# Optimization experiments

Measured on AMD Instinct MI355X. Metric: run time of the kernel, lower is better.

Reference implementation:

```python
import jax, jax.numpy as jnp
import numpy as np
from jax import lax

B, T, D = 2048, 300, 40
H = 64          # BasicLSTMCell num_units
D1 = 128        # dense1 units
OUT = 512       # out_dim (num speakers)
FORGET_BIAS = 1.0
BN_EPS = 1e-3   # tf.layers.BatchNormalization default


def setup_inputs() -> dict:
    key = jax.random.key(0)
    ks = jax.random.split(key, 10)
    X = jax.random.normal(ks[0], (B, T, D), dtype=jnp.float32)
    seq_length = jax.random.randint(ks[1], (B,), 1, T + 1).astype(jnp.int32)
    # BasicLSTMCell kernel: [input_dim + H, 4H], gate order i, j, f, o
    lstm_kernel = jax.random.normal(ks[2], (D + H, 4 * H), dtype=jnp.float32) * 0.08
    lstm_bias = jnp.zeros((4 * H,), dtype=jnp.float32)
    W1 = jax.random.normal(ks[3], (H, D1), dtype=jnp.float32) * 0.1
    b1 = jnp.zeros((D1,), dtype=jnp.float32)
    gamma = jnp.ones((D1,), dtype=jnp.float32)
    beta = jnp.zeros((D1,), dtype=jnp.float32)
    moving_mean = jnp.zeros((D1,), dtype=jnp.float32)
    moving_var = jnp.ones((D1,), dtype=jnp.float32)
    W2 = jax.random.normal(ks[4], (D1, OUT), dtype=jnp.float32) * 0.1
    b2 = jnp.zeros((OUT,), dtype=jnp.float32)
    return {"X": X, "seq_length": seq_length,
            "lstm_kernel": lstm_kernel, "lstm_bias": lstm_bias,
            "W1": W1, "b1": b1, "gamma": gamma, "beta": beta,
            "moving_mean": moving_mean, "moving_var": moving_var,
            "W2": W2, "b2": b2}


def reference(X, seq_length, lstm_kernel, lstm_bias, W1, b1, gamma, beta,
              moving_mean, moving_var, W2, b2):
    b = X.shape[0]
    c0 = jnp.zeros((b, H), dtype=X.dtype)
    h0 = jnp.zeros((b, H), dtype=X.dtype)

    def step(carry, x_t):
        c, h = carry
        z = jnp.concatenate([x_t, h], axis=1) @ lstm_kernel + lstm_bias
        i, j, f, o = jnp.split(z, 4, axis=1)
        new_c = c * jax.nn.sigmoid(f + FORGET_BIAS) + jax.nn.sigmoid(i) * jnp.tanh(j)
        new_h = jnp.tanh(new_c) * jax.nn.sigmoid(o)
        return (new_c, new_h), new_h

    _, outs = lax.scan(step, (c0, h0), jnp.swapaxes(X, 0, 1))  # [T, B, H]
    outs = jnp.swapaxes(outs, 0, 1)  # [B, T, H]

    # gather last valid timestep per sample
    idx = (seq_length - 1).astype(jnp.int32)
    final = jnp.take_along_axis(outs, idx[:, None, None], axis=1)[:, 0, :]  # [B, H]

    x = jax.nn.relu(final @ W1 + b1)
    # BatchNorm in inference mode (training=False): use moving statistics
    x = gamma * (x - moving_mean) * lax.rsqrt(moving_var + BN_EPS) + beta
    return jax.nn.softmax(x @ W2 + b2, axis=-1)
```

## Files before the change

### kernel.cpp

```cpp
#include <hip/hip_runtime.h>
#include <stdint.h>

#define TT 300
#define DD 40
#define SB 8
#define AROW 200
#define ZROW 260

typedef __attribute__((ext_vector_type(8))) short short8;
typedef __attribute__((ext_vector_type(4))) float f32x4;

__device__ __forceinline__ ushort f2bf(float f) {
  uint32_t b = __float_as_uint(f);
  b += 0x7FFFu + ((b >> 16) & 1u);
  return (ushort)(b >> 16);
}
__device__ __forceinline__ float sigm(float x) {
  return __builtin_amdgcn_rcpf(1.0f + __expf(-x));
}
__device__ __forceinline__ float tanh_f(float x) {
  return 1.0f - 2.0f * __builtin_amdgcn_rcpf(1.0f + __expf(2.0f * x));
}

__global__ __launch_bounds__(256, 1) void lstm_mfma_kernel(
    const float* __restrict__ X, const int* __restrict__ seqlen,
    const float* __restrict__ Wk, const float* __restrict__ bias,
    float* __restrict__ hfin)
{
  __shared__ ushort wstage[64 * 128];
  __shared__ ushort Ash[16 * AROW];
  __shared__ float zbuf[8 * ZROW];

  const int tid = threadIdx.x;
  const int wv = tid >> 6, lane = tid & 63;
  const int s0 = blockIdx.x * SB;

  for (int i = tid; i < 16 * AROW; i += 256) Ash[i] = 0;

  short8 Bf[6][4];
  for (int c = 0; c < 4; ++c) {
    __syncthreads();
    for (int i = tid; i < 64 * 128; i += 256) {
      int kp = i >> 6, cc = i & 63;
      ushort v = 0;
      int ks = (kp < 40) ? kp : ((kp >= 64) ? (kp - 24) : -1);
      if (ks >= 0) {
        int u = c * 16 + (cc >> 2), g = cc & 3;
        v = f2bf(Wk[ks * 256 + g * 64 + u]);
      }
      wstage[cc * 128 + kp] = v;
    }
    __syncthreads();
    if (wv == c) {
      #pragma unroll
      for (int kt = 0; kt < 6; ++kt) {
        int kk = ((kt < 4) ? kt * 32 : (kt * 32 - 64)) + (lane >> 4) * 8;
        #pragma unroll
        for (int nt = 0; nt < 4; ++nt) {
          int cc = nt * 16 + (lane & 15);
          Bf[kt][nt] = *reinterpret_cast<const short8*>(&wstage[cc * 128 + kk]);
        }
      }
    }
  }

  const int ps = tid >> 5;
  const int u0 = (2 * tid) & 63, u1 = u0 + 1;
  const int mylen = seqlen[s0 + ps];
  const float bi0 = bias[u0],      bj0 = bias[64 + u0];
  const float bfg0 = bias[128 + u0] + 1.0f, bo0 = bias[192 + u0];
  const float bi1 = bias[u1],      bj1 = bias[64 + u1];
  const float bfg1 = bias[128 + u1] + 1.0f, bo1 = bias[192 + u1];

  int ml = seqlen[s0 + (lane & 7)];
  #pragma unroll
  for (int off = 1; off < 64; off <<= 1) ml = max(ml, __shfl_xor(ml, off));

  const int iA = tid, iB = 256 + tid;
  const int sA = (iA * 205) >> 13, dA = iA - sA * 40;
  int sB = (iB * 205) >> 13; if (sB > 7) sB = 7;
  const int dB = iB - sB * 40;
  const float* xpA = X + (size_t)(s0 + sA) * (TT * DD) + dA;
  const float* xpB = X + (size_t)(s0 + sB) * (TT * DD) + dB;
  const bool hasB = (iB < SB * DD);

  Ash[sA * AROW + dA] = f2bf(xpA[0]);
  if (hasB) Ash[sB * AROW + dB] = f2bf(xpB[0]);
  __syncthreads();

  float c0 = 0.f, c1 = 0.f, hf0 = 0.f, hf1 = 0.f;

  for (int t = 0; t < ml; ++t) {
    short8 Af[6];
    #pragma unroll
    for (int kt = 0; kt < 6; ++kt)
      Af[kt] = *reinterpret_cast<const short8*>(
          &Ash[(lane & 15) * AROW + kt * 32 + (lane >> 4) * 8]);

    const bool pre = (t + 1 < ml);
    float xnA = 0.f, xnB = 0.f;
    if (pre) {
      xnA = xpA[(t + 1) * DD];
      if (hasB) xnB = xpB[(t + 1) * DD];
    }

    f32x4 zero4 = {0.f, 0.f, 0.f, 0.f};
    f32x4 acc[4] = {zero4, zero4, zero4, zero4};
    #pragma unroll
    for (int kt = 0; kt < 6; ++kt) {
      #pragma unroll
      for (int nt = 0; nt < 4; ++nt)
        acc[nt] = __builtin_amdgcn_mfma_f32_16x16x32_bf16(Af[kt], Bf[kt][nt], acc[nt], 0, 0, 0);
    }

    if (lane < 32) {
      const int q = lane >> 4, cl = lane & 15;
      #pragma unroll
      for (int nt = 0; nt < 4; ++nt) {
        #pragma unroll
        for (int r = 0; r < 4; ++r)
          zbuf[(q * 4 + r) * ZROW + wv * 64 + nt * 16 + cl] = acc[nt][r];
      }
    }
    __syncthreads();

    f32x4 z0 = *reinterpret_cast<const f32x4*>(&zbuf[ps * ZROW + u0 * 4]);
    f32x4 z1 = *reinterpret_cast<const f32x4*>(&zbuf[ps * ZROW + u1 * 4]);
    float nc0 = c0 * sigm(z0[2] + bfg0) + sigm(z0[0] + bi0) * tanh_f(z0[1] + bj0);
    float nh0 = tanh_f(nc0) * sigm(z0[3] + bo0);
    float nc1 = c1 * sigm(z1[2] + bfg1) + sigm(z1[0] + bi1) * tanh_f(z1[1] + bj1);
    float nh1 = tanh_f(nc1) * sigm(z1[3] + bo1);
    c0 = nc0; c1 = nc1;
    if (t == mylen - 1) { hf0 = nh0; hf1 = nh1; }

    ushort hh0 = f2bf(nh0);
    ushort hl0 = f2bf(nh0 - __uint_as_float((uint32_t)hh0 << 16));
    ushort hh1 = f2bf(nh1);
    ushort hl1 = f2bf(nh1 - __uint_as_float((uint32_t)hh1 << 16));
    Ash[ps * AROW + 64 + u0] = hh0;
    Ash[ps * AROW + 128 + u0] = hl0;
    Ash[ps * AROW + 64 + u1] = hh1;
    Ash[ps * AROW + 128 + u1] = hl1;
    if (pre) {
      Ash[sA * AROW + dA] = f2bf(xnA);
      if (hasB) Ash[sB * AROW + dB] = f2bf(xnB);
    }
    __syncthreads();
  }

  hfin[(size_t)(s0 + ps) * 64 + u0] = hf0;
  hfin[(size_t)(s0 + ps) * 64 + u1] = hf1;
}

__global__ __launch_bounds__(256, 1) void head_kernel(
    const float* __restrict__ hfin,
    const float* __restrict__ W1, const float* __restrict__ b1,
    const float* __restrict__ gamma, const float* __restrict__ beta,
    const float* __restrict__ mmean, const float* __restrict__ mvar,
    const float* __restrict__ W2, const float* __restrict__ b2,
    float* __restrict__ out)
{
  __shared__ float hl[16 * 64];
  __shared__ float d1t[128 * 20];
  __shared__ float lg[16 * 516];
  const int tid = threadIdx.x;
  const int b0 = blockIdx.x * 16;

  for (int i = tid; i < 16 * 64; i += 256) hl[i] = hfin[(size_t)b0 * 64 + i];
  __syncthreads();

  {
    const int j = tid & 127, sg = tid >> 7;
    float acc[8];
    const float bb = b1[j];
    #pragma unroll
    for (int s = 0; s < 8; ++s) acc[s] = bb;
    for (int k = 0; k < 64; ++k) {
      float w = W1[k * 128 + j];
      #pragma unroll
      for (int s = 0; s < 8; ++s) acc[s] = fmaf(hl[(sg * 8 + s) * 64 + k], w, acc[s]);
    }
    const float ga = gamma[j], be = beta[j], mm = mmean[j];
    const float iv = rsqrtf(mvar[j] + 1e-3f);
    #pragma unroll
    for (int s = 0; s < 8; ++s) {
      float v = fmaxf(acc[s], 0.f);
      d1t[j * 20 + sg * 8 + s] = ga * (v - mm) * iv + be;
    }
  }
  __syncthreads();

  {
    const int cA = tid * 2;
    float accA[16], accB[16];
    const float bA = b2[cA], bB = b2[cA + 1];
    #pragma unroll
    for (int s = 0; s < 16; ++s) { accA[s] = bA; accB[s] = bB; }
    for (int k = 0; k < 128; ++k) {
      const float2 w = *reinterpret_cast<const float2*>(&W2[k * 512 + cA]);
      const f32x4 dq0 = *reinterpret_cast<const f32x4*>(&d1t[k * 20]);
      const f32x4 dq1 = *reinterpret_cast<const f32x4*>(&d1t[k * 20 + 4]);
      const f32x4 dq2 = *reinterpret_cast<const f32x4*>(&d1t[k * 20 + 8]);
      const f32x4 dq3 = *reinterpret_cast<const f32x4*>(&d1t[k * 20 + 12]);
      #pragma unroll
      for (int s = 0; s < 4; ++s) {
        accA[s]      = fmaf(dq0[s], w.x, accA[s]);      accB[s]      = fmaf(dq0[s], w.y, accB[s]);
        accA[s + 4]  = fmaf(dq1[s], w.x, accA[s + 4]);  accB[s + 4]  = fmaf(dq1[s], w.y, accB[s + 4]);
        accA[s + 8]  = fmaf(dq2[s], w.x, accA[s + 8]);  accB[s + 8]  = fmaf(dq2[s], w.y, accB[s + 8]);
        accA[s + 12] = fmaf(dq3[s], w.x, accA[s + 12]); accB[s + 12] = fmaf(dq3[s], w.y, accB[s + 12]);
      }
    }
    #pragma unroll
    for (int s = 0; s < 16; ++s) {
      lg[s * 516 + cA]     = accA[s];
      lg[s * 516 + cA + 1] = accB[s];
    }
  }
  __syncthreads();

  {
    const int w = tid >> 6, lane = tid & 63;
    #pragma unroll
    for (int si = 0; si < 4; ++si) {
      const int s = w * 4 + si;
      float v[8];
      float m = -3.4e38f;
      #pragma unroll
      for (int i = 0; i < 8; ++i) { v[i] = lg[s * 516 + lane + 64 * i]; m = fmaxf(m, v[i]); }
      #pragma unroll
      for (int off = 1; off < 64; off <<= 1) m = fmaxf(m, __shfl_xor(m, off));
      float sum = 0.f;
      #pragma unroll
      for (int i = 0; i < 8; ++i) { v[i] = __expf(v[i] - m); sum += v[i]; }
      #pragma unroll
      for (int off = 1; off < 64; off <<= 1) sum += __shfl_xor(sum, off);
      const float inv = __builtin_amdgcn_rcpf(sum);
      #pragma unroll
      for (int i = 0; i < 8; ++i)
        out[(size_t)(b0 + s) * 512 + lane + 64 * i] = v[i] * inv;
    }
  }
}

extern "C" void kernel_launch(void* const* d_in, const int* in_sizes, int n_in,
                              void* d_out, int out_size, void* d_ws, size_t ws_size,
                              hipStream_t stream) {
  const float* X      = (const float*)d_in[0];
  const int*   seqlen = (const int*)d_in[1];
  const float* Wk     = (const float*)d_in[2];
  const float* bias   = (const float*)d_in[3];
  const float* W1     = (const float*)d_in[4];
  const float* b1     = (const float*)d_in[5];
  const float* gam    = (const float*)d_in[6];
  const float* bet    = (const float*)d_in[7];
  const float* mmean  = (const float*)d_in[8];
  const float* mvar   = (const float*)d_in[9];
  const float* W2     = (const float*)d_in[10];
  const float* b2     = (const float*)d_in[11];
  float* out  = (float*)d_out;
  float* hfin = (float*)d_ws;

  lstm_mfma_kernel<<<dim3(256), dim3(256), 0, stream>>>(X, seqlen, Wk, bias, hfin);
  head_kernel<<<dim3(128), dim3(256), 0, stream>>>(hfin, W1, b1, gam, bet,
                                                   mmean, mvar, W2, b2, out);
}
```

Baseline: 427.5 us.

## Fuse LSTM and head into one kernel with 4 samples per block

Merges the LSTM recurrence and the dense/BN/softmax head into one kernel launched over 512 blocks of 4 samples each, so all 256 CUs get work. The A operand is double-buffered, which removes one block barrier per timestep; the z exchange now stays within a wave and waits only on LDS. X rows are prefetched four steps ahead into registers. The head matmuls move into the same block through a shared-memory union, which removes the hfin round trip and the second launch. Each block still loads and converts all the weights, and each MFMA tile uses only 4 of its 16 rows, so compute per sample goes up.

After: 506.5 us. +18.5%, slower.

```diff
diff --git a/kernel.cpp b/kernel.cpp
--- a/kernel.cpp
+++ b/kernel.cpp
@@ -3,242 +3,227 @@
 
 #define TT 300
 #define DD 40
-#define SB 8
 #define AROW 200
 #define ZROW 260
 
 typedef __attribute__((ext_vector_type(8))) short short8;
 typedef __attribute__((ext_vector_type(4))) float f32x4;
+
+union SMemU {
+  ushort wstage[64 * 128];
+  struct {
+    ushort Abuf[2][16 * AROW];
+    float  zbuf[4 * ZROW];
+  } s;
+  struct {
+    float lg[4 * 512];
+    float d1t[128 * 4];
+    float hbuf[4 * 64];
+  } h;
+};
 
 __device__ __forceinline__ ushort f2bf(float f) {
   uint32_t b = __float_as_uint(f);
   b += 0x7FFFu + ((b >> 16) & 1u);
   return (ushort)(b >> 16);
 }
+__device__ __forceinline__ float bf2f(ushort h) {
+  return __uint_as_float((uint32_t)h << 16);
+}
 __device__ __forceinline__ float sigm(float x) {
   return __builtin_amdgcn_rcpf(1.0f + __expf(-x));
 }
 __device__ __forceinline__ float tanh_f(float x) {
   return 1.0f - 2.0f * __builtin_amdgcn_rcpf(1.0f + __expf(2.0f * x));
 }
-
-__global__ __launch_bounds__(256, 1) void lstm_mfma_kernel(
+__device__ __forceinline__ void block_sync_lds() {
+  asm volatile("s_waitcnt lgkmcnt(0)" ::: "memory");
+  __builtin_amdgcn_s_barrier();
+}
+
+__global__ __launch_bounds__(256, 2) void lstm_fused_kernel(
     const float* __restrict__ X, const int* __restrict__ seqlen,
     const float* __restrict__ Wk, const float* __restrict__ bias,
-    float* __restrict__ hfin)
-{
-  __shared__ ushort wstage[64 * 128];
-  __shared__ ushort Ash[16 * AROW];
-  __shared__ float zbuf[8 * ZROW];
-
-  const int tid = threadIdx.x;
-  const int wv = tid >> 6, lane = tid & 63;
-  const int s0 = blockIdx.x * SB;
-
-  for (int i = tid; i < 16 * AROW; i += 256) Ash[i] = 0;
-
-  short8 Bf[6][4];
-  for (int c = 0; c < 4; ++c) {
-    __syncthreads();
-    for (int i = tid; i < 64 * 128; i += 256) {
-      int kp = i >> 6, cc = i & 63;
-      ushort v = 0;
-      int ks = (kp < 40) ? kp : ((kp >= 64) ? (kp - 24) : -1);
-      if (ks >= 0) {
-        int u = c * 16 + (cc >> 2), g = cc & 3;
-        v = f2bf(Wk[ks * 256 + g * 64 + u]);
-      }
-      wstage[cc * 128 + kp] = v;
-    }
-    __syncthreads();
-    if (wv == c) {
-      #pragma unroll
-      for (int kt = 0; kt < 6; ++kt) {
-        int kk = ((kt < 4) ? kt * 32 : (kt * 32 - 64)) + (lane >> 4) * 8;
-        #pragma unroll
-        for (int nt = 0; nt < 4; ++nt) {
-          int cc = nt * 16 + (lane & 15);
-          Bf[kt][nt] = *reinterpret_cast<const short8*>(&wstage[cc * 128 + kk]);
-        }
-      }
-    }
-  }
-
-  const int ps = tid >> 5;
-  const int u0 = (2 * tid) & 63, u1 = u0 + 1;
-  const int mylen = seqlen[s0 + ps];
-  const float bi0 = bias[u0],      bj0 = bias[64 + u0];
-  const float bfg0 = bias[128 + u0] + 1.0f, bo0 = bias[192 + u0];
-  const float bi1 = bias[u1],      bj1 = bias[64 + u1];
-  const float bfg1 = bias[128 + u1] + 1.0f, bo1 = bias[192 + u1];
-
-  int ml = seqlen[s0 + (lane & 7)];
-  #pragma unroll
-  for (int off = 1; off < 64; off <<= 1) ml = max(ml, __shfl_xor(ml, off));
-
-  const int iA = tid, iB = 256 + tid;
-  const int sA = (iA * 205) >> 13, dA = iA - sA * 40;
-  int sB = (iB * 205) >> 13; if (sB > 7) sB = 7;
-  const int dB = iB - sB * 40;
-  const float* xpA = X + (size_t)(s0 + sA) * (TT * DD) + dA;
-  const float* xpB = X + (size_t)(s0 + sB) * (TT * DD) + dB;
-  const bool hasB = (iB < SB * DD);
-
-  Ash[sA * AROW + dA] = f2bf(xpA[0]);
-  if (hasB) Ash[sB * AROW + dB] = f2bf(xpB[0]);
-  __syncthreads();
-
-  float c0 = 0.f, c1 = 0.f, hf0 = 0.f, hf1 = 0.f;
-
-  for (int t = 0; t < ml; ++t) {
-    short8 Af[6];
-    #pragma unroll
-    for (int kt = 0; kt < 6; ++kt)
-      Af[kt] = *reinterpret_cast<const short8*>(
-          &Ash[(lane & 15) * AROW + kt * 32 + (lane >> 4) * 8]);
-
-    const bool pre = (t + 1 < ml);
-    float xnA = 0.f, xnB = 0.f;
-    if (pre) {
-      xnA = xpA[(t + 1) * DD];
-      if (hasB) xnB = xpB[(t + 1) * DD];
-    }
-
-    f32x4 zero4 = {0.f, 0.f, 0.f, 0.f};
-    f32x4 acc[4] = {zero4, zero4, zero4, zero4};
-    #pragma unroll
-    for (int kt = 0; kt < 6; ++kt) {
-      #pragma unroll
-      for (int nt = 0; nt < 4; ++nt)
-        acc[nt] = __builtin_amdgcn_mfma_f32_16x16x32_bf16(Af[kt], Bf[kt][nt], acc[nt], 0, 0, 0);
-    }
-
-    if (lane < 32) {
-      const int q = lane >> 4, cl = lane & 15;
-      #pragma unroll
-      for (int nt = 0; nt < 4; ++nt) {
-        #pragma unroll
-        for (int r = 0; r < 4; ++r)
-          zbuf[(q * 4 + r) * ZROW + wv * 64 + nt * 16 + cl] = acc[nt][r];
-      }
-    }
-    __syncthreads();
-
-    f32x4 z0 = *reinterpret_cast<const f32x4*>(&zbuf[ps * ZROW + u0 * 4]);
-    f32x4 z1 = *reinterpret_cast<const f32x4*>(&zbuf[ps * ZROW + u1 * 4]);
-    float nc0 = c0 * sigm(z0[2] + bfg0) + sigm(z0[0] + bi0) * tanh_f(z0[1] + bj0);
-    float nh0 = tanh_f(nc0) * sigm(z0[3] + bo0);
-    float nc1 = c1 * sigm(z1[2] + bfg1) + sigm(z1[0] + bi1) * tanh_f(z1[1] + bj1);
-    float nh1 = tanh_f(nc1) * sigm(z1[3] + bo1);
-    c0 = nc0; c1 = nc1;
-    if (t == mylen - 1) { hf0 = nh0; hf1 = nh1; }
-
-    ushort hh0 = f2bf(nh0);
-    ushort hl0 = f2bf(nh0 - __uint_as_float((uint32_t)hh0 << 16));
-    ushort hh1 = f2bf(nh1);
-    ushort hl1 = f2bf(nh1 - __uint_as_float((uint32_t)hh1 << 16));
-    Ash[ps * AROW + 64 + u0] = hh0;
-    Ash[ps * AROW + 128 + u0] = hl0;
-    Ash[ps * AROW + 64 + u1] = hh1;
-    Ash[ps * AROW + 128 + u1] = hl1;
-    if (pre) {
-      Ash[sA * AROW + dA] = f2bf(xnA);
-      if (hasB) Ash[sB * AROW + dB] = f2bf(xnB);
-    }
-    __syncthreads();
-  }
-
-  hfin[(size_t)(s0 + ps) * 64 + u0] = hf0;
-  hfin[(size_t)(s0 + ps) * 64 + u1] = hf1;
-}
-
-__global__ __launch_bounds__(256, 1) void head_kernel(
-    const float* __restrict__ hfin,
     const float* __restrict__ W1, const float* __restrict__ b1,
     const float* __restrict__ gamma, const float* __restrict__ beta,
     const float* __restrict__ mmean, const float* __restrict__ mvar,
     const float* __restrict__ W2, const float* __restrict__ b2,
     float* __restrict__ out)
 {
-  __shared__ float hl[16 * 64];
-  __shared__ float d1t[128 * 20];
-  __shared__ float lg[16 * 516];
+  __shared__ SMemU sm;
   const int tid = threadIdx.x;
-  const int b0 = blockIdx.x * 16;
-
-  for (int i = tid; i < 16 * 64; i += 256) hl[i] = hfin[(size_t)b0 * 64 + i];
+  const int wv = tid >> 6, lane = tid & 63;
+  const int s0 = blockIdx.x * 4;
+
+  short8 Bf[6][4];
+  for (int c = 0; c < 4; ++c) {
+    __syncthreads();
+    for (int i = tid; i < 64 * 128; i += 256) {
+      int cc = i >> 7, kp = i & 127;
+      ushort v = 0;
+      int ks = (kp < 40) ? kp : ((kp >= 64) ? (kp - 24) : -1);
+      if (ks >= 0) {
+        int u = c * 16 + (cc >> 2), g = cc & 3;
+        v = f2bf(Wk[ks * 256 + g * 64 + u]);
+      }
+      sm.wstage[cc * 128 + kp] = v;
+    }
+    __syncthreads();
+    if (wv == c) {
+      #pragma unroll
+      for (int kt = 0; kt < 6; ++kt) {
+        int kk = ((kt < 4) ? kt * 32 : (kt * 32 - 64)) + (lane >> 4) * 8;
+        #pragma unroll
+        for (int nt = 0; nt < 4; ++nt)
+          Bf[kt][nt] = *reinterpret_cast<const short8*>(
+              &sm.wstage[(nt * 16 + (lane & 15)) * 128 + kk]);
+      }
+    }
+  }
   __syncthreads();
 
   {
-    const int j = tid & 127, sg = tid >> 7;
-    float acc[8];
-    const float bb = b1[j];
-    #pragma unroll
-    for (int s = 0; s < 8; ++s) acc[s] = bb;
+    uint32_t* az = reinterpret_cast<uint32_t*>(&sm.s.Abuf[0][0]);
+    for (int i = tid; i < 2 * 16 * AROW / 2; i += 256) az[i] = 0;
+  }
+  __syncthreads();
+
+  const int ps = lane >> 4;
+  const int u  = wv * 16 + (lane & 15);
+  const int mylen = seqlen[s0 + ps];
+  const float bi = bias[u], bj = bias[64 + u];
+  const float bfp = bias[128 + u] + 1.0f, bo = bias[192 + u];
+
+  int ml = seqlen[s0 + (lane & 3)];
+  #pragma unroll
+  for (int off = 1; off < 64; off <<= 1) ml = max(ml, __shfl_xor(ml, off));
+  ml = __builtin_amdgcn_readfirstlane(ml);
+
+  const int sA = (tid * 205) >> 13;
+  const int dA = tid - sA * 40;
+  const bool xth = (tid < 160);
+  const float* xp = X + (size_t)(s0 + sA) * (TT * DD) + dA;
+
+  float xr[4];
+  if (xth) {
+    sm.s.Abuf[0][sA * AROW + dA] = f2bf(xp[0]);
+    #pragma unroll
+    for (int j = 1; j <= 4; ++j) xr[j & 3] = xp[j * DD];
+  }
+  __syncthreads();
+
+  float cst = 0.f, hf = 0.f;
+
+  for (int t = 0; t < ml; ++t) {
+    const int p = t & 1;
+    const ushort* Ab = &sm.s.Abuf[p][0];
+    short8 Af[6];
+    #pragma unroll
+    for (int kt = 0; kt < 6; ++kt)
+      Af[kt] = *reinterpret_cast<const short8*>(
+          &Ab[(lane & 15) * AROW + kt * 32 + (lane >> 4) * 8]);
+
+    f32x4 zero4 = {0.f, 0.f, 0.f, 0.f};
+    f32x4 acc[4] = {zero4, zero4, zero4, zero4};
+    #pragma unroll
+    for (int kt = 0; kt < 6; ++kt) {
+      #pragma unroll
+      for (int nt = 0; nt < 4; ++nt)
+        acc[nt] = __builtin_amdgcn_mfma_f32_16x16x32_bf16(Af[kt], Bf[kt][nt], acc[nt], 0, 0, 0);
+    }
+
+    if (lane < 16) {
+      #pragma unroll
+      for (int nt = 0; nt < 4; ++nt) {
+        #pragma unroll
+        for (int r = 0; r < 4; ++r)
+          sm.s.zbuf[r * ZROW + wv * 64 + nt * 16 + lane] = acc[nt][r];
+      }
+    }
+    asm volatile("s_waitcnt lgkmcnt(0)" ::: "memory");
+
+    f32x4 z = *reinterpret_cast<const f32x4*>(
+        &sm.s.zbuf[ps * ZROW + wv * 64 + 4 * (lane & 15)]);
+    float nc = cst * sigm(z[2] + bfp) + sigm(z[0] + bi) * tanh_f(z[1] + bj);
+    float nh = tanh_f(nc) * sigm(z[3] + bo);
+    cst = nc;
+    if (t == mylen - 1) hf = nh;
+
+    ushort* An = &sm.s.Abuf[1 - p][0];
+    ushort hh = f2bf(nh);
+    An[ps * AROW + 64 + u] = hh;
+    An[ps * AROW + 128 + u] = f2bf(nh - bf2f(hh));
+    if (xth) {
+      An[sA * AROW + dA] = f2bf(xr[(t + 1) & 3]);
+      float nv = 0.f;
+      if (t + 5 < TT) nv = xp[(t + 5) * DD];
+      xr[(t + 1) & 3] = nv;
+    }
+    block_sync_lds();
+  }
+
+  sm.h.hbuf[ps * 64 + u] = hf;
+  block_sync_lds();
+
+  {
+    const int j = tid & 127, sp = tid >> 7;
+    float a0 = b1[j], a1 = a0;
     for (int k = 0; k < 64; ++k) {
       float w = W1[k * 128 + j];
-      #pragma unroll
-      for (int s = 0; s < 8; ++s) acc[s] = fmaf(hl[(sg * 8 + s) * 64 + k], w, acc[s]);
+      a0 = fmaf(sm.h.hbuf[sp * 64 + k], w, a0);
+      a1 = fmaf(sm.h.hbuf[(sp + 2) * 64 + k], w, a1);
     }
     const float ga = gamma[j], be = beta[j], mm = mmean[j];
     const float iv = rsqrtf(mvar[j] + 1e-3f);
-    #pragma unroll
-    for (int s = 0; s < 8; ++s) {
-      float v = fmaxf(acc[s], 0.f);
-      d1t[j * 20 + sg * 8 + s] = ga * (v - mm) * iv + be;
-    }
-  }
-  __syncthreads();
+    a0 = fmaxf(a0, 0.f); a1 = fmaxf(a1, 0.f);
+    sm.h.d1t[j * 4 + sp]     = ga * (a0 - mm) * iv + be;
+    sm.h.d1t[j * 4 + sp + 2] = ga * (a1 - mm) * iv + be;
+  }
+  block_sync_lds();
 
   {
     const int cA = tid * 2;
-    float accA[16], accB[16];
+    float ax[4], ay[4];
     const float bA = b2[cA], bB = b2[cA + 1];
     #pragma unroll
-    for (int s = 0; s < 16; ++s) { accA[s] = bA; accB[s] = bB; }
+    for (int s = 0; s < 4; ++s) { ax[s] = bA; ay[s] = bB; }
+    #pragma unroll 4
     for (int k = 0; k < 128; ++k) {
       const float2 w = *reinterpret_cast<const float2*>(&W2[k * 512 + cA]);
-      const f32x4 dq0 = *reinterpret_cast<const f32x4*>(&d1t[k * 20]);
-      const f32x4 dq1 = *reinterpret_cast<const f32x4*>(&d1t[k * 20 + 4]);
-      const f32x4 dq2 = *reinterpret_cast<const f32x4*>(&d1t[k * 20 + 8]);
-      const f32x4 dq3 = *reinterpret_cast<const f32x4*>(&d1t[k * 20 + 12]);
+      const f32x4 d = *reinterpret_cast<const f32x4*>(&sm.h.d1t[k * 4]);
       #pragma unroll
       for (int s = 0; s < 4; ++s) {
-        accA[s]      = fmaf(dq0[s], w.x, accA[s]);      accB[s]      = fmaf(dq0[s], w.y, accB[s]);
-        accA[s + 4]  = fmaf(dq1[s], w.x, accA[s + 4]);  accB[s + 4]  = fmaf(dq1[s], w.y, accB[s + 4]);
-        accA[s + 8]  = fmaf(dq2[s], w.x, accA[s + 8]);  accB[s + 8]  = fmaf(dq2[s], w.y, accB[s + 8]);
-        accA[s + 12] = fmaf(dq3[s], w.x, accA[s + 12]); accB[s + 12] = fmaf(dq3[s], w.y, accB[s + 12]);
-      }
-    }
-    #pragma unroll
-    for (int s = 0; s < 16; ++s) {
-      lg[s * 516 + cA]     = accA[s];
-      lg[s * 516 + cA + 1] = accB[s];
-    }
-  }
-  __syncthreads();
-
-  {
-    const int w = tid >> 6, lane = tid & 63;
-    #pragma unroll
-    for (int si = 0; si < 4; ++si) {
-      const int s = w * 4 + si;
-      float v[8];
-      float m = -3.4e38f;
-      #pragma unroll
-      for (int i = 0; i < 8; ++i) { v[i] = lg[s * 516 + lane + 64 * i]; m = fmaxf(m, v[i]); }
-      #pragma unroll
-      for (int off = 1; off < 64; off <<= 1) m = fmaxf(m, __shfl_xor(m, off));
-      float sum = 0.f;
-      #pragma unroll
-      for (int i = 0; i < 8; ++i) { v[i] = __expf(v[i] - m); sum += v[i]; }
-      #pragma unroll
-      for (int off = 1; off < 64; off <<= 1) sum += __shfl_xor(sum, off);
-      const float inv = __builtin_amdgcn_rcpf(sum);
-      #pragma unroll
-      for (int i = 0; i < 8; ++i)
-        out[(size_t)(b0 + s) * 512 + lane + 64 * i] = v[i] * inv;
-    }
+        ax[s] = fmaf(d[s], w.x, ax[s]);
+        ay[s] = fmaf(d[s], w.y, ay[s]);
+      }
+    }
+    #pragma unroll
+    for (int s = 0; s < 4; ++s) {
+      float2 lw = make_float2(ax[s], ay[s]);
+      *reinterpret_cast<float2*>(&sm.h.lg[s * 512 + cA]) = lw;
+    }
+  }
+  block_sync_lds();
+
+  {
+    float v[8];
+    float m = -3.4e38f;
+    #pragma unroll
+    for (int i = 0; i < 8; ++i) {
+      v[i] = sm.h.lg[wv * 512 + lane + 64 * i];
+      m = fmaxf(m, v[i]);
+    }
+    #pragma unroll
+    for (int off = 1; off < 64; off <<= 1) m = fmaxf(m, __shfl_xor(m, off));
+    float sum = 0.f;
+    #pragma unroll
+    for (int i = 0; i < 8; ++i) { v[i] = __expf(v[i] - m); sum += v[i]; }
+    #pragma unroll
+    for (int off = 1; off < 64; off <<= 1) sum += __shfl_xor(sum, off);
+    const float inv = __builtin_amdgcn_rcpf(sum);
+    #pragma unroll
+    for (int i = 0; i < 8; ++i)
+      out[(size_t)(s0 + wv) * 512 + lane + 64 * i] = v[i] * inv;
   }
 }
 
@@ -257,10 +242,8 @@
   const float* mvar   = (const float*)d_in[9];
   const float* W2     = (const float*)d_in[10];
   const float* b2     = (const float*)d_in[11];
-  float* out  = (float*)d_out;
-  float* hfin = (float*)d_ws;
-
-  lstm_mfma_kernel<<<dim3(256), dim3(256), 0, stream>>>(X, seqlen, Wk, bias, hfin);
-  head_kernel<<<dim3(128), dim3(256), 0, stream>>>(hfin, W1, b1, gam, bet,
-                                                   mmean, mvar, W2, b2, out);
-}
+  float* out = (float*)d_out;
+
+  lstm_fused_kernel<<<dim3(512), dim3(256), 0, stream>>>(
+      X, seqlen, Wk, bias, W1, b1, gam, bet, mmean, mvar, W2, b2, out);
+}
```
